# Kernel optimization log

Measured on AMD Instinct MI355X. Metric: run time of the kernel, lower is better.

## Reference

```python
import jax, jax.numpy as jnp
import numpy as np

IMG = 1024.0
MAXD = 8.0
EPS = 1e-6
ENC_HEADS = 12
DEC_HEADS = 16


def _ln(x, w, b):
    m = jnp.mean(x, -1, keepdims=True)
    v = jnp.mean((x - m) ** 2, -1, keepdims=True)
    return (x - m) / jnp.sqrt(v + EPS) * w + b


def _attn(x, qkv_w, qkv_b, pr_w, pr_b, nh, key_mask):
    B, L, D = x.shape
    hd = D // nh
    qkv = (x @ qkv_w + qkv_b).reshape(B, L, 3, nh, hd).transpose(2, 0, 3, 1, 4)
    q, k, v = qkv[0], qkv[1], qkv[2]  # [B, nh, L, hd]
    s = jnp.einsum('bhqd,bhkd->bhqk', q, k) * (hd ** -0.5)
    if key_mask is not None:
        # restrict attention to visible tokens; identical math to per-sample gather+encode
        s = jnp.where(key_mask[:, None, None, :], s, -1e9)
    a = jax.nn.softmax(s, -1)
    o = jnp.einsum('bhqk,bhkd->bhqd', a, v).transpose(0, 2, 1, 3).reshape(B, L, D)
    return o @ pr_w + pr_b


def _block(x, i, ln1w, ln1b, qkvw, qkvb, prw, prb, ln2w, ln2b, f1w, f1b, f2w, f2b, nh, key_mask):
    x = x + _attn(_ln(x, ln1w[i], ln1b[i]), qkvw[i], qkvb[i], prw[i], prb[i], nh, key_mask)
    h = jax.nn.gelu(_ln(x, ln2w[i], ln2b[i]) @ f1w[i] + f1b[i], approximate=False)
    return x + h @ f2w[i] + f2b[i]


def _pos(coords, depths, w1, b1, w2, b2):
    x1, x2, y1, y2 = coords[..., 0], coords[..., 1], coords[..., 2], coords[..., 3]
    f = jnp.stack([(x1 + x2) / 2.0 / IMG, (y1 + y2) / 2.0 / IMG,
                   (x2 - x1) / IMG, (y2 - y1) / IMG, depths / MAXD], -1)
    return jax.nn.gelu(f @ w1 + b1, approximate=False) @ w2 + b2


def _forward(patches, coords, depths, pe_w, pe_b, pos1_w, pos1_b, pos2_w, pos2_b,
             e_ln1_w, e_ln1_b, e_qkv_w, e_qkv_b, e_pr_w, e_pr_b, e_ln2_w, e_ln2_b,
             e_f1_w, e_f1_b, e_f2_w, e_f2_b, enorm_w, enorm_b,
             de_w, de_b, mask_token, dpos1_w, dpos1_b, dpos2_w, dpos2_b,
             d_ln1_w, d_ln1_b, d_qkv_w, d_qkv_b, d_pr_w, d_pr_b, d_ln2_w, d_ln2_b,
             d_f1_w, d_f1_b, d_f2_w, d_f2_b, dnorm_w, dnorm_b,
             hi_w, hi_b, hn_w, hn_b, mask):
    B, L = mask.shape
    x = patches.reshape(B, L, -1) @ pe_w + pe_b + _pos(coords, depths, pos1_w, pos1_b, pos2_w, pos2_b)
    visible = (mask == 0)
    h = x
    for i in range(e_qkv_w.shape[0]):
        h = _block(h, i, e_ln1_w, e_ln1_b, e_qkv_w, e_qkv_b, e_pr_w, e_pr_b,
                   e_ln2_w, e_ln2_b, e_f1_w, e_f1_b, e_f2_w, e_f2_b, ENC_HEADS, visible)
    encoded = jnp.where(visible[..., None], _ln(h, enorm_w, enorm_b), 0.0)
    xd = encoded @ de_w + de_b
    xd = jnp.where((mask != 0)[..., None], mask_token, xd)
    xd = xd + _pos(coords, depths, dpos1_w, dpos1_b, dpos2_w, dpos2_b)
    for i in range(d_qkv_w.shape[0]):
        xd = _block(xd, i, d_ln1_w, d_ln1_b, d_qkv_w, d_qkv_b, d_pr_w, d_pr_b,
                    d_ln2_w, d_ln2_b, d_f1_w, d_f1_b, d_f2_w, d_f2_b, DEC_HEADS, None)
    xd = _ln(xd, dnorm_w, dnorm_b)
    return (xd @ hi_w + hi_b, xd @ hn_w + hn_b)


def setup_inputs() -> dict:
    key = jax.random.key(0)
    ks = iter(jax.random.split(key, 80))
    def nrm(shape, std=0.02):
        return jax.random.normal(next(ks), shape, jnp.float32) * std
    B, L, P, C = 4, 512, 32, 1
    D, DD = 768, 512
    ED, DDEP = 12, 8
    pd = C * P * P
    inp = {}
    inp['patches'] = jax.random.normal(next(ks), (B, L, C, P, P), jnp.float32)
    inp['coords'] = jax.random.uniform(next(ks), (B, L, 4), jnp.float32)
    inp['depths'] = jax.random.uniform(next(ks), (B, L), jnp.float32)
    inp['mask'] = jax.random.randint(next(ks), (B, L), 0, 2, jnp.int32)
    inp['pe_w'] = nrm((pd, D)); inp['pe_b'] = jnp.zeros((D,))
    inp['pos1_w'] = nrm((5, D // 2)); inp['pos1_b'] = jnp.zeros((D // 2,))
    inp['pos2_w'] = nrm((D // 2, D)); inp['pos2_b'] = jnp.zeros((D,))
    inp['e_ln1_w'] = jnp.ones((ED, D)); inp['e_ln1_b'] = jnp.zeros((ED, D))
    inp['e_qkv_w'] = nrm((ED, D, 3 * D)); inp['e_qkv_b'] = jnp.zeros((ED, 3 * D))
    inp['e_pr_w'] = nrm((ED, D, D)); inp['e_pr_b'] = jnp.zeros((ED, D))
    inp['e_ln2_w'] = jnp.ones((ED, D)); inp['e_ln2_b'] = jnp.zeros((ED, D))
    inp['e_f1_w'] = nrm((ED, D, 4 * D)); inp['e_f1_b'] = jnp.zeros((ED, 4 * D))
    inp['e_f2_w'] = nrm((ED, 4 * D, D)); inp['e_f2_b'] = jnp.zeros((ED, D))
    inp['enorm_w'] = jnp.ones((D,)); inp['enorm_b'] = jnp.zeros((D,))
    inp['de_w'] = nrm((D, DD)); inp['de_b'] = jnp.zeros((DD,))
    inp['mask_token'] = nrm((DD,))
    inp['dpos1_w'] = nrm((5, DD // 2)); inp['dpos1_b'] = jnp.zeros((DD // 2,))
    inp['dpos2_w'] = nrm((DD // 2, DD)); inp['dpos2_b'] = jnp.zeros((DD,))
    inp['d_ln1_w'] = jnp.ones((DDEP, DD)); inp['d_ln1_b'] = jnp.zeros((DDEP, DD))
    inp['d_qkv_w'] = nrm((DDEP, DD, 3 * DD)); inp['d_qkv_b'] = jnp.zeros((DDEP, 3 * DD))
    inp['d_pr_w'] = nrm((DDEP, DD, DD)); inp['d_pr_b'] = jnp.zeros((DDEP, DD))
    inp['d_ln2_w'] = jnp.ones((DDEP, DD)); inp['d_ln2_b'] = jnp.zeros((DDEP, DD))
    inp['d_f1_w'] = nrm((DDEP, DD, 4 * DD)); inp['d_f1_b'] = jnp.zeros((DDEP, 4 * DD))
    inp['d_f2_w'] = nrm((DDEP, 4 * DD, DD)); inp['d_f2_b'] = jnp.zeros((DDEP, DD))
    inp['dnorm_w'] = jnp.ones((DD,)); inp['dnorm_b'] = jnp.zeros((DD,))
    inp['hi_w'] = nrm((DD, pd)); inp['hi_b'] = jnp.zeros((pd,))
    inp['hn_w'] = nrm((DD, pd)); inp['hn_b'] = jnp.zeros((pd,))
    return inp


def reference(patches, coords, depths, pe_w, pe_b, pos1_w, pos1_b, pos2_w, pos2_b,
              e_ln1_w, e_ln1_b, e_qkv_w, e_qkv_b, e_pr_w, e_pr_b, e_ln2_w, e_ln2_b,
              e_f1_w, e_f1_b, e_f2_w, e_f2_b, enorm_w, enorm_b,
              de_w, de_b, mask_token, dpos1_w, dpos1_b, dpos2_w, dpos2_b,
              d_ln1_w, d_ln1_b, d_qkv_w, d_qkv_b, d_pr_w, d_pr_b, d_ln2_w, d_ln2_b,
              d_f1_w, d_f1_b, d_f2_w, d_f2_b, dnorm_w, dnorm_b,
              hi_w, hi_b, hn_w, hn_b, mask):
    return _forward(patches, coords, depths, pe_w, pe_b, pos1_w, pos1_b, pos2_w, pos2_b,
                    e_ln1_w, e_ln1_b, e_qkv_w, e_qkv_b, e_pr_w, e_pr_b, e_ln2_w, e_ln2_b,
                    e_f1_w, e_f1_b, e_f2_w, e_f2_b, enorm_w, enorm_b,
                    de_w, de_b, mask_token, dpos1_w, dpos1_b, dpos2_w, dpos2_b,
                    d_ln1_w, d_ln1_b, d_qkv_w, d_qkv_b, d_pr_w, d_pr_b, d_ln2_w, d_ln2_b,
                    d_f1_w, d_f1_b, d_f2_w, d_f2_b, dnorm_w, dnorm_b,
                    hi_w, hi_b, hn_w, hn_b, mask)
```

## Files before the change

kernel.cpp:

```cpp
#include <hip/hip_runtime.h>
#include <hip/hip_bf16.h>

using bf16 = __hip_bfloat16;
typedef __bf16 bf16x8 __attribute__((ext_vector_type(8)));
typedef float f32x4 __attribute__((ext_vector_type(4)));

__device__ __forceinline__ float gelu_exact(float x) {
    return 0.5f * x * (1.0f + erff(x * 0.70710678118654752440f));
}

#define GLD_LDS16(g, l) __builtin_amdgcn_global_load_lds( \
    (__attribute__((address_space(1))) void*)(g),          \
    (__attribute__((address_space(3))) void*)(l), 16, 0, 0)

#define WAITV(n) asm volatile("s_waitcnt vmcnt(" #n ")" ::: "memory")

template<int BM,int BN,int WM,int WN,int FM,int FN,int OUT_BF16,int HAS_BIAS,int HAS_RES,int DO_GELU,int HEADS,int MPA,int OCC>
__global__ __launch_bounds__(256, OCC) void gemm_bt(
    const bf16* __restrict__ A, long lda,
    const bf16* __restrict__ Bt, long ldb,
    void* __restrict__ Cv, long ldc,
    const float* __restrict__ bias, const float* __restrict__ Res,
    int K, float alpha,
    const int* __restrict__ mpa_mask, const float* __restrict__ mpa_tok,
    const float* __restrict__ mpa_pos)
{
    static_assert(WM * WN == 4 && BM == WM * FM * 16 && BN == WN * FN * 16, "cfg");
    __shared__ alignas(16) unsigned short As[4][BM * 32];
    __shared__ alignas(16) unsigned short Bs[4][BN * 32];

    const int nwg = gridDim.x * gridDim.y;
    const int orig = blockIdx.y * gridDim.x + blockIdx.x;
    const int q = nwg >> 3, r = nwg & 7;
    const int xcd = orig & 7, seq = orig >> 3;
    const int wg = (xcd < r ? xcd * (q + 1) : r * (q + 1) + (xcd - r) * q) + seq;
    const int bn0 = (wg % gridDim.x) * BN;
    const int bm0 = (wg / gridDim.x) * BM;

    const int tid = threadIdx.x;
    const int wave = tid >> 6, lane = tid & 63;
    const int wm = (wave / WN) * (FM * 16);
    const int wn = (wave % WN) * (FN * 16);

    f32x4 acc[FM][FN] = {};

    constexpr int CA = BM / 16, CT = (BM + BN) / 16;
    constexpr int LPT = CT / 4;
    static_assert(CT % 4 == 0 && (LPT == 2 || LPT == 3), "stage cfg");
    const int lrow = lane >> 2;
    const int lcol = (((lane & 3) ^ ((lrow >> 1) & 3)) * 8);
    const int nk = K >> 5;

    const int fr = lane & 15;
    const int kg = lane >> 4;
    const int kswz = (kg ^ ((fr >> 1) & 3)) * 8;

    auto stage = [&](int buf, int kt) {
        const int k0 = kt * 32;
        for (int c = wave; c < CT; c += 4) {
            if (c < CA) {
                const bf16* src = A + (long)(bm0 + c * 16 + lrow) * lda + k0 + lcol;
                GLD_LDS16(src, &As[buf][c * 512]);
            } else {
                const int c2 = c - CA;
                const bf16* src = Bt + (long)(bn0 + c2 * 16 + lrow) * ldb + k0 + lcol;
                GLD_LDS16(src, &Bs[buf][c2 * 512]);
            }
        }
    };

    for (int i = 0; i < 4 && i < nk; ++i) stage(i, i);

    for (int t0 = 0; t0 < nk; t0 += 2) {
        const int c = (nk - t0 >= 2) ? 2 : 1;
        const int staged = (t0 + 4 < nk) ? (t0 + 4) : nk;
        const int extra = staged - (t0 + c);
        if constexpr (LPT == 2) {
            switch (extra) { case 2: WAITV(4); break; case 1: WAITV(2); break;
                             default: WAITV(0); }
        } else {
            switch (extra) { case 2: WAITV(6); break; case 1: WAITV(3); break;
                             default: WAITV(0); }
        }
        __builtin_amdgcn_s_barrier();
        __builtin_amdgcn_sched_barrier(0);

        #pragma unroll
        for (int u = 0; u < 2; ++u) {
            if (u == 1 && c == 1) break;
            const int cur = (t0 + u) & 3;
            bf16x8 af[FM], bfv[FN];
            #pragma unroll
            for (int m = 0; m < FM; ++m)
                af[m] = *(const bf16x8*)&As[cur][(wm + m * 16 + fr) * 32 + kswz];
            #pragma unroll
            for (int n = 0; n < FN; ++n)
                bfv[n] = *(const bf16x8*)&Bs[cur][(wn + n * 16 + fr) * 32 + kswz];
            __builtin_amdgcn_s_setprio(1);
            #pragma unroll
            for (int m = 0; m < FM; ++m)
                #pragma unroll
                for (int n = 0; n < FN; ++n)
                    acc[m][n] = __builtin_amdgcn_mfma_f32_16x16x32_bf16(af[m], bfv[n], acc[m][n], 0, 0, 0);
            __builtin_amdgcn_s_setprio(0);
        }

        __builtin_amdgcn_sched_barrier(0);
        asm volatile("s_waitcnt lgkmcnt(0)" ::: "memory");
        __builtin_amdgcn_s_barrier();
        if (t0 + 4 < nk) stage((t0 + 4) & 3, t0 + 4);
        if (t0 + 5 < nk) stage((t0 + 5) & 3, t0 + 5);
    }

    const int r0 = (lane >> 4) * 4;
    #pragma unroll
    for (int m = 0; m < FM; ++m) {
        const int rowb = bm0 + wm + m * 16 + r0;
        #pragma unroll
        for (int n = 0; n < FN; ++n) {
            const int col = bn0 + wn + n * 16 + fr;
            #pragma unroll
            for (int j = 0; j < 4; ++j) {
                float v = acc[m][n][j] * alpha;
                if (HEADS) {
                    v += (col < 1024) ? bias[col] : ((const float*)Res)[col - 1024];
                    const long idx = (col < 1024)
                        ? (long)(rowb + j) * 1024 + col
                        : 2097152L + (long)(rowb + j) * 1024 + (col - 1024);
                    ((float*)Cv)[idx] = v;
                    continue;
                }
                if (MPA) {
                    const int row = rowb + j;
                    v += bias[col];
                    if (mpa_mask[row] != 0) v = mpa_tok[col];
                    v += mpa_pos[(long)row * ldc + col];
                    ((float*)Cv)[(long)row * ldc + col] = v;
                    continue;
                }
                if (HAS_BIAS) v += bias[col];
                if (HAS_RES)  v += Res[(long)(rowb + j) * ldc + col];
                if (DO_GELU)  v = gelu_exact(v);
                const long idx = (long)(rowb + j) * ldc + col;
                if (OUT_BF16) ((bf16*)Cv)[idx] = __float2bfloat16(v);
                else          ((float*)Cv)[idx] = v;
            }
        }
    }
}

#define GEMM_A(OB,HB,HR,DG) gemm_bt<64,128,2,2,2,4, OB,HB,HR,DG,0,0,3>
#define GEMM_B(OB,HB,HR,DG) gemm_bt<64,64,2,2,2,2, OB,HB,HR,DG,0,0,4>
#define GEMM_H              gemm_bt<64,64,2,2,2,2, 0,1,0,0,1,0,4>
#define GEMM_M              gemm_bt<64,64,2,2,2,2, 0,1,0,0,0,1,4>

template<int HD, int MASKED>
__global__ __launch_bounds__(256) void flash_attn(
    const bf16* __restrict__ qkv, int ldq, int Doff, int nh,
    bf16* __restrict__ Out, int ldo,
    const int* __restrict__ mask, float alpha)
{
    constexpr int KVT = 256, KS = HD + 8, SV = KVT + 8;
    __shared__ unsigned short Ks[KVT * KS];
    __shared__ unsigned short Vs[HD * SV];
    __shared__ unsigned short Pl[4][16 * 40];

    const int bh = blockIdx.y, b = bh / nh, h = bh % nh;
    const int tid = threadIdx.x;
    const int wave = tid >> 6, lane = tid & 63;
    const int q0 = blockIdx.x * 64 + wave * 16;
    const int fr = lane & 15, kg = lane >> 4;

    const bf16* Qb = qkv + ((long)(b * 512 + q0 + fr)) * ldq + h * HD;
    bf16x8 af[HD / 32];
    #pragma unroll
    for (int kc = 0; kc < HD / 32; ++kc)
        af[kc] = *(const bf16x8*)(Qb + kc * 32 + kg * 8);

    const bf16* Kg = qkv + (long)b * 512 * ldq + Doff + h * HD;
    const bf16* Vg = qkv + (long)b * 512 * ldq + 2 * Doff + h * HD;
    const int* mg = mask + (long)b * 512;

    float m[4], l[4];
    f32x4 O[HD / 16] = {};
    #pragma unroll
    for (int j = 0; j < 4; ++j) { m[j] = -INFINITY; l[j] = 0.f; }

    for (int t = 0; t < 512; t += KVT) {
        __syncthreads();
        for (int i = tid; i < KVT * (HD / 8); i += 256) {
            const int rr = i / (HD / 8), c = i % (HD / 8);
            *(bf16x8*)&Ks[rr * KS + c * 8] = *(const bf16x8*)(Kg + (long)(t + rr) * ldq + c * 8);
        }
        for (int i = tid; i < KVT * (HD / 8); i += 256) {
            const int ll = i / (HD / 8), c = i % (HD / 8);
            bf16x8 vv = *(const bf16x8*)(Vg + (long)(t + ll) * ldq + c * 8);
            #pragma unroll
            for (int j = 0; j < 8; ++j) {
                bf16 e = ((const bf16*)&vv)[j];
                Vs[(c * 8 + j) * SV + ll] = *(unsigned short*)&e;
            }
        }
        __syncthreads();

        for (int n0 = 0; n0 < KVT; n0 += 32) {
            f32x4 s[2];
            int msk[2] = {0, 0};
            #pragma unroll
            for (int f = 0; f < 2; ++f) {
                f32x4 a = {};
                __builtin_amdgcn_s_setprio(1);
                #pragma unroll
                for (int kc = 0; kc < HD / 32; ++kc) {
                    bf16x8 kb = *(const bf16x8*)&Ks[(n0 + f * 16 + fr) * KS + kc * 32 + kg * 8];
                    a = __builtin_amdgcn_mfma_f32_16x16x32_bf16(af[kc], kb, a, 0, 0, 0);
                }
                __builtin_amdgcn_s_setprio(0);
                #pragma unroll
                for (int j = 0; j < 4; ++j) a[j] *= alpha;
                s[f] = a;
                if (MASKED) msk[f] = mg[t + n0 + f * 16 + fr];
            }
            float g[4], p0[4], p1[4];
            #pragma unroll
            for (int j = 0; j < 4; ++j) {
                float t4 = fmaxf(s[0][j], s[1][j]);
                t4 = fmaxf(t4, __shfl_xor(t4, 1));
                t4 = fmaxf(t4, __shfl_xor(t4, 2));
                t4 = fmaxf(t4, __shfl_xor(t4, 4));
                t4 = fmaxf(t4, __shfl_xor(t4, 8));
                const float mn = fmaxf(m[j], t4);
                g[j] = __expf(m[j] - mn);
                p0[j] = msk[0] ? 0.f : __expf(s[0][j] - mn);
                p1[j] = msk[1] ? 0.f : __expf(s[1][j] - mn);
                float rs = p0[j] + p1[j];
                rs += __shfl_xor(rs, 1);
                rs += __shfl_xor(rs, 2);
                rs += __shfl_xor(rs, 4);
                rs += __shfl_xor(rs, 8);
                l[j] = l[j] * g[j] + rs;
                m[j] = mn;
            }
            #pragma unroll
            for (int dt = 0; dt < HD / 16; ++dt)
                #pragma unroll
                for (int j = 0; j < 4; ++j) O[dt][j] *= g[j];
            unsigned short* pl = &Pl[wave][0];
            #pragma unroll
            for (int j = 0; j < 4; ++j) {
                bf16 b0 = __float2bfloat16(p0[j]);
                bf16 b1 = __float2bfloat16(p1[j]);
                pl[(kg * 4 + j) * 40 + fr]      = *(unsigned short*)&b0;
                pl[(kg * 4 + j) * 40 + 16 + fr] = *(unsigned short*)&b1;
            }
            __builtin_amdgcn_sched_barrier(0);
            bf16x8 pa = *(const bf16x8*)&pl[fr * 40 + kg * 8];
            __builtin_amdgcn_s_setprio(1);
            #pragma unroll
            for (int dt = 0; dt < HD / 16; ++dt) {
                bf16x8 vb = *(const bf16x8*)&Vs[(dt * 16 + fr) * SV + n0 + kg * 8];
                O[dt] = __builtin_amdgcn_mfma_f32_16x16x32_bf16(pa, vb, O[dt], 0, 0, 0);
            }
            __builtin_amdgcn_s_setprio(0);
        }
    }

    float inv[4];
    #pragma unroll
    for (int j = 0; j < 4; ++j) inv[j] = 1.0f / l[j];
    #pragma unroll
    for (int dt = 0; dt < HD / 16; ++dt)
        #pragma unroll
        for (int j = 0; j < 4; ++j) {
            const long row = (long)b * 512 + q0 + kg * 4 + j;
            Out[row * ldo + h * HD + dt * 16 + fr] = __float2bfloat16(O[dt][j] * inv[j]);
        }
}

__global__ void transpose_cast_b(const float* __restrict__ in, bf16* __restrict__ out,
                                 int K, int N, int Kpad, long inS, long outS)
{
    __shared__ float tile[32][33];
    in  += (long)blockIdx.z * inS;
    out += (long)blockIdx.z * outS;
    const int n0 = blockIdx.x * 32, k0 = blockIdx.y * 32;
    const int tx = threadIdx.x & 31, ty = threadIdx.x >> 5;
    #pragma unroll
    for (int r = 0; r < 4; ++r) {
        const int k = k0 + ty + r * 8, n = n0 + tx;
        tile[ty + r * 8][tx] = (k < K && n < N) ? in[(long)k * N + n] : 0.0f;
    }
    __syncthreads();
    #pragma unroll
    for (int r = 0; r < 4; ++r) {
        const int n = n0 + ty + r * 8, k = k0 + tx;
        if (n < N && k < Kpad)
            out[(long)n * Kpad + k] = __float2bfloat16(tile[tx][ty + r * 8]);
    }
}

template<int Dd, int MASKED>
__global__ __launch_bounds__(256) void ln_wave(
    const float* __restrict__ X, const float* __restrict__ w, const float* __restrict__ b,
    bf16* __restrict__ Y, const int* __restrict__ mask)
{
    const int wave = threadIdx.x >> 6, lane = threadIdx.x & 63;
    const int t = blockIdx.x * 4 + wave;
    const float* x = X + (long)t * Dd;
    constexpr int NE = Dd / 64;
    float v[NE];
    float s = 0.f, s2 = 0.f;
    #pragma unroll
    for (int k = 0; k < NE; ++k) {
        v[k] = x[lane + k * 64];
        s += v[k]; s2 += v[k] * v[k];
    }
    #pragma unroll
    for (int o = 32; o; o >>= 1) { s += __shfl_xor(s, o); s2 += __shfl_xor(s2, o); }
    const float mean = s / Dd;
    const float var = s2 / Dd - mean * mean;
    const float inv = 1.0f / sqrtf(var + 1e-6f);
    const bool zero = MASKED && (mask[t] != 0);
    #pragma unroll
    for (int k = 0; k < NE; ++k) {
        const int c = lane + k * 64;
        const float rr = zero ? 0.0f : ((v[k] - mean) * inv * w[c] + b[c]);
        Y[(long)t * Dd + c] = __float2bfloat16(rr);
    }
}

__global__ void build_feat(const float* __restrict__ coords, const float* __restrict__ depths,
                           bf16* __restrict__ F)
{
    const int t = blockIdx.x * 256 + threadIdx.x;
    if (t >= 2048) return;
    const float* c = coords + t * 4;
    float f[5];
    f[0] = (c[0] + c[1]) * 0.5f / 1024.0f;
    f[1] = (c[2] + c[3]) * 0.5f / 1024.0f;
    f[2] = (c[1] - c[0]) / 1024.0f;
    f[3] = (c[3] - c[2]) / 1024.0f;
    f[4] = depths[t] / 8.0f;
    bf16* o = F + (long)t * 32;
    #pragma unroll
    for (int j = 0; j < 32; ++j)
        o[j] = __float2bfloat16(j < 5 ? f[j] : 0.0f);
}

__global__ void conv_patches(const float* __restrict__ in, bf16* __restrict__ out, int n)
{
    const int i = blockIdx.x * 256 + threadIdx.x;
    if (i < n) out[i] = __float2bfloat16(in[i]);
}

extern "C" void kernel_launch(void* const* d_in, const int* in_sizes, int n_in,
                              void* d_out, int out_size, void* d_ws, size_t ws_size,
                              hipStream_t stream)
{
    (void)in_sizes; (void)n_in; (void)out_size;
    const int D = 768, DD = 512;

    const float* patches    = (const float*)d_in[0];
    const float* coords     = (const float*)d_in[1];
    const float* depths     = (const float*)d_in[2];
    const int*   mask       = (const int*)d_in[3];
    const float* pe_w       = (const float*)d_in[4];
    const float* pe_b       = (const float*)d_in[5];
    const float* pos1_w     = (const float*)d_in[6];
    const float* pos1_b     = (const float*)d_in[7];
    const float* pos2_w     = (const float*)d_in[8];
    const float* pos2_b     = (const float*)d_in[9];
    const float* e_ln1_w    = (const float*)d_in[10];
    const float* e_ln1_b    = (const float*)d_in[11];
    const float* e_qkv_w    = (const float*)d_in[12];
    const float* e_qkv_b    = (const float*)d_in[13];
    const float* e_pr_w     = (const float*)d_in[14];
    const float* e_pr_b     = (const float*)d_in[15];
    const float* e_ln2_w    = (const float*)d_in[16];
    const float* e_ln2_b    = (const float*)d_in[17];
    const float* e_f1_w     = (const float*)d_in[18];
    const float* e_f1_b     = (const float*)d_in[19];
    const float* e_f2_w     = (const float*)d_in[20];
    const float* e_f2_b     = (const float*)d_in[21];
    const float* enorm_w    = (const float*)d_in[22];
    const float* enorm_b    = (const float*)d_in[23];
    const float* de_w       = (const float*)d_in[24];
    const float* de_b       = (const float*)d_in[25];
    const float* mask_token = (const float*)d_in[26];
    const float* dpos1_w    = (const float*)d_in[27];
    const float* dpos1_b    = (const float*)d_in[28];
    const float* dpos2_w    = (const float*)d_in[29];
    const float* dpos2_b    = (const float*)d_in[30];
    const float* d_ln1_w    = (const float*)d_in[31];
    const float* d_ln1_b    = (const float*)d_in[32];
    const float* d_qkv_w    = (const float*)d_in[33];
    const float* d_qkv_b    = (const float*)d_in[34];
    const float* d_pr_w     = (const float*)d_in[35];
    const float* d_pr_b     = (const float*)d_in[36];
    const float* d_ln2_w    = (const float*)d_in[37];
    const float* d_ln2_b    = (const float*)d_in[38];
    const float* d_f1_w     = (const float*)d_in[39];
    const float* d_f1_b     = (const float*)d_in[40];
    const float* d_f2_w     = (const float*)d_in[41];
    const float* d_f2_b     = (const float*)d_in[42];
    const float* dnorm_w    = (const float*)d_in[43];
    const float* dnorm_b    = (const float*)d_in[44];
    const float* hi_w       = (const float*)d_in[45];
    const float* hi_b       = (const float*)d_in[46];
    const float* hn_w       = (const float*)d_in[47];
    const float* hn_b       = (const float*)d_in[48];

    char* p = (char*)d_ws;
    auto alloc = [&](size_t bytes) -> char* {
        char* r = p; p += (bytes + 255) & ~(size_t)255; return r;
    };
    bf16* pe_wt  = (bf16*)alloc(768L * 1024 * 2);
    bf16* pos1t  = (bf16*)alloc(384L * 32 * 2);
    bf16* pos2t  = (bf16*)alloc(768L * 384 * 2);
    bf16* dpos1t = (bf16*)alloc(256L * 32 * 2);
    bf16* dpos2t = (bf16*)alloc(512L * 256 * 2);
    bf16* de_t   = (bf16*)alloc(512L * 768 * 2);
    bf16* hi_t   = (bf16*)alloc(1024L * 512 * 2);
    bf16* hn_t   = (bf16*)alloc(1024L * 512 * 2);
    bf16* wslot  = (bf16*)alloc(3072L * 768 * 2);
    bf16*  feat    = (bf16*)alloc(2048L * 32 * 2);
    bf16*  patchbf = (bf16*)alloc(2048L * 1024 * 2);
    bf16*  poshE   = (bf16*)alloc(2048L * 384 * 2);
    float* posE    = (float*)alloc(2048L * 768 * 4);
    bf16*  poshD   = (bf16*)alloc(2048L * 256 * 2);
    float* posD    = (float*)alloc(2048L * 512 * 4);
    float* xbuf    = (float*)alloc(2048L * 768 * 4);
    bf16*  lnbuf   = (bf16*)alloc(2048L * 768 * 2);
    bf16*  qkvbuf  = (bf16*)alloc(2048L * 2304 * 2);
    bf16*  hid     = (bf16*)alloc(2048L * 3072 * 2);
    bf16*  pin     = (bf16*)alloc(2048L * 768 * 2);
    float* xd      = (float*)alloc(2048L * 512 * 4);

    const size_t bigBytes =
        (12L*2304*768 + 12L*768*768 + 12L*3072*768 + 12L*768*3072 +
          8L*1536*512 +  8L*512*512 +  8L*2048*512 +  8L*512*2048) * 2 + 8 * 256;
    const size_t used = (size_t)(p - (char*)d_ws);
    const bool batched = ws_size >= used + bigBytes;
    bf16 *eqkvt = nullptr, *eprt = nullptr, *ef1t = nullptr, *ef2t = nullptr;
    bf16 *dqkvt = nullptr, *dprt = nullptr, *df1t = nullptr, *df2t = nullptr;
    if (batched) {
        eqkvt = (bf16*)alloc(12L * 2304 * 768 * 2);
        eprt  = (bf16*)alloc(12L * 768 * 768 * 2);
        ef1t  = (bf16*)alloc(12L * 3072 * 768 * 2);
        ef2t  = (bf16*)alloc(12L * 768 * 3072 * 2);
        dqkvt = (bf16*)alloc(8L * 1536 * 512 * 2);
        dprt  = (bf16*)alloc(8L * 512 * 512 * 2);
        df1t  = (bf16*)alloc(8L * 2048 * 512 * 2);
        df2t  = (bf16*)alloc(8L * 512 * 2048 * 2);
    }

    conv_patches<<<8192, 256, 0, stream>>>(patches, patchbf, 2097152);
    build_feat<<<8, 256, 0, stream>>>(coords, depths, feat);

    auto trb = [&](const float* in, bf16* out, int K, int N, int Kpad, int z) {
        dim3 g((N + 31) / 32, (Kpad + 31) / 32, z);
        transpose_cast_b<<<g, 256, 0, stream>>>(in, out, K, N, Kpad, (long)K * N, (long)N * Kpad);
    };
    trb(pe_w,    pe_wt,  1024,  768, 1024, 1);
    trb(pos1_w,  pos1t,     5,  384,   32, 1);
    trb(pos2_w,  pos2t,   384,  768,  384, 1);
    trb(dpos1_w, dpos1t,    5,  256,   32, 1);
    trb(dpos2_w, dpos2t,  256,  512,  256, 1);
    trb(de_w,    de_t,    768,  512,  768, 1);
    trb(hi_w,    hi_t,    512, 1024,  512, 1);
    trb(hn_w,    hn_t,    512, 1024,  512, 1);
    if (batched) {
        trb(e_qkv_w, eqkvt, 768, 2304, 768, 12);
        trb(e_pr_w,  eprt,  768,  768, 768, 12);
        trb(e_f1_w,  ef1t,  768, 3072, 768, 12);
        trb(e_f2_w,  ef2t, 3072,  768, 3072, 12);
        trb(d_qkv_w, dqkvt, 512, 1536, 512, 8);
        trb(d_pr_w,  dprt,  512,  512, 512, 8);
        trb(d_f1_w,  df1t,  512, 2048, 512, 8);
        trb(d_f2_w,  df2t, 2048,  512, 2048, 8);
    }
    auto wsl = [&](const float* src, long off, int K, int N, int Kpad) -> const bf16* {
        dim3 g((N + 31) / 32, (Kpad + 31) / 32, 1);
        transpose_cast_b<<<g, 256, 0, stream>>>(src + off, wslot, K, N, Kpad, 0, 0);
        return wslot;
    };

    GEMM_B(1,1,0,1)<<<dim3(6,32,1),256,0,stream>>>(
        feat, 32, pos1t, 32, poshE, 384, pos1_b, nullptr, 32, 1.0f, nullptr, nullptr, nullptr);
    GEMM_B(0,1,0,0)<<<dim3(12,32,1),256,0,stream>>>(
        poshE, 384, pos2t, 384, posE, 768, pos2_b, nullptr, 384, 1.0f, nullptr, nullptr, nullptr);
    GEMM_B(1,1,0,1)<<<dim3(4,32,1),256,0,stream>>>(
        feat, 32, dpos1t, 32, poshD, 256, dpos1_b, nullptr, 32, 1.0f, nullptr, nullptr, nullptr);
    GEMM_B(0,1,0,0)<<<dim3(8,32,1),256,0,stream>>>(
        poshD, 256, dpos2t, 256, posD, 512, dpos2_b, nullptr, 256, 1.0f, nullptr, nullptr, nullptr);

    GEMM_B(0,1,1,0)<<<dim3(12,32,1),256,0,stream>>>(
        patchbf, 1024, pe_wt, 1024, xbuf, 768, pe_b, posE, 1024, 1.0f, nullptr, nullptr, nullptr);

    for (int i = 0; i < 12; ++i) {
        ln_wave<768,0><<<512,256,0,stream>>>(xbuf, e_ln1_w + i*D, e_ln1_b + i*D, lnbuf, nullptr);
        const bf16* Wq = batched ? eqkvt + (long)i*2304*768
                                 : wsl(e_qkv_w, (long)i*768*2304, 768, 2304, 768);
        GEMM_A(1,1,0,0)<<<dim3(18,32,1),256,0,stream>>>(
            lnbuf, 768, Wq, 768, qkvbuf, 2304, e_qkv_b + i*2304, nullptr, 768, 1.0f, nullptr, nullptr, nullptr);
        flash_attn<64,1><<<dim3(8,48),256,0,stream>>>(
            qkvbuf, 2304, 768, 12, pin, 768, mask, 0.125f);
        const bf16* Wp = batched ? eprt + (long)i*768*768
                                 : wsl(e_pr_w, (long)i*768*768, 768, 768, 768);
        GEMM_B(0,1,1,0)<<<dim3(12,32,1),256,0,stream>>>(
            pin, 768, Wp, 768, xbuf, 768, e_pr_b + i*768, xbuf, 768, 1.0f, nullptr, nullptr, nullptr);
        ln_wave<768,0><<<512,256,0,stream>>>(xbuf, e_ln2_w + i*D, e_ln2_b + i*D, lnbuf, nullptr);
        const bf16* W1 = batched ? ef1t + (long)i*3072*768
                                 : wsl(e_f1_w, (long)i*768*3072, 768, 3072, 768);
        GEMM_A(1,1,0,1)<<<dim3(24,32,1),256,0,stream>>>(
            lnbuf, 768, W1, 768, hid, 3072, e_f1_b + i*3072, nullptr, 768, 1.0f, nullptr, nullptr, nullptr);
        const bf16* W2 = batched ? ef2t + (long)i*768*3072
                                 : wsl(e_f2_w, (long)i*3072*768, 3072, 768, 3072);
        GEMM_B(0,1,1,0)<<<dim3(12,32,1),256,0,stream>>>(
            hid, 3072, W2, 3072, xbuf, 768, e_f2_b + i*768, xbuf, 3072, 1.0f, nullptr, nullptr, nullptr);
    }

    ln_wave<768,1><<<512,256,0,stream>>>(xbuf, enorm_w, enorm_b, lnbuf, mask);
    GEMM_M<<<dim3(8,32,1),256,0,stream>>>(
        lnbuf, 768, de_t, 768, xd, 512, de_b, nullptr, 768, 1.0f, mask, mask_token, posD);

    for (int i = 0; i < 8; ++i) {
        ln_wave<512,0><<<512,256,0,stream>>>(xd, d_ln1_w + i*DD, d_ln1_b + i*DD, lnbuf, nullptr);
        const bf16* Wq = batched ? dqkvt + (long)i*1536*512
                                 : wsl(d_qkv_w, (long)i*512*1536, 512, 1536, 512);
        GEMM_A(1,1,0,0)<<<dim3(12,32,1),256,0,stream>>>(
            lnbuf, 512, Wq, 512, qkvbuf, 1536, d_qkv_b + i*1536, nullptr, 512, 1.0f, nullptr, nullptr, nullptr);
        flash_attn<32,0><<<dim3(8,64),256,0,stream>>>(
            qkvbuf, 1536, 512, 16, pin, 512, nullptr, 0.17677669529663687f);
        const bf16* Wp = batched ? dprt + (long)i*512*512
                                 : wsl(d_pr_w, (long)i*512*512, 512, 512, 512);
        GEMM_B(0,1,1,0)<<<dim3(8,32,1),256,0,stream>>>(
            pin, 512, Wp, 512, xd, 512, d_pr_b + i*512, xd, 512, 1.0f, nullptr, nullptr, nullptr);
        ln_wave<512,0><<<512,256,0,stream>>>(xd, d_ln2_w + i*DD, d_ln2_b + i*DD, lnbuf, nullptr);
        const bf16* W1 = batched ? df1t + (long)i*2048*512
                                 : wsl(d_f1_w, (long)i*512*2048, 512, 2048, 512);
        GEMM_A(1,1,0,1)<<<dim3(16,32,1),256,0,stream>>>(
            lnbuf, 512, W1, 512, hid, 2048, d_f1_b + i*2048, nullptr, 512, 1.0f, nullptr, nullptr, nullptr);
        const bf16* W2 = batched ? df2t + (long)i*512*2048
                                 : wsl(d_f2_w, (long)i*2048*512, 2048, 512, 2048);
        GEMM_B(0,1,1,0)<<<dim3(8,32,1),256,0,stream>>>(
            hid, 2048, W2, 2048, xd, 512, d_f2_b + i*512, xd, 2048, 1.0f, nullptr, nullptr, nullptr);
    }

    ln_wave<512,0><<<512,256,0,stream>>>(xd, dnorm_w, dnorm_b, lnbuf, nullptr);
    GEMM_H<<<dim3(32,32,1),256,0,stream>>>(
        lnbuf, 512, hi_t, 512, (float*)d_out, 1024, hi_b, (const float*)hn_b, 512, 1.0f, nullptr, nullptr, nullptr);
}
```

Measured before the change: 2.838 ms.

## Split-K residual GEMMs with atomic accumulation into residual stream

```diff
diff --git a/kernel.cpp b/kernel.cpp
--- a/kernel.cpp
+++ b/kernel.cpp
@@ -15,7 +15,7 @@
 
 #define WAITV(n) asm volatile("s_waitcnt vmcnt(" #n ")" ::: "memory")
 
-template<int BM,int BN,int WM,int WN,int FM,int FN,int OUT_BF16,int HAS_BIAS,int HAS_RES,int DO_GELU,int HEADS,int MPA,int OCC>
+template<int BM,int BN,int WM,int WN,int FM,int FN,int OUT_BF16,int HAS_BIAS,int HAS_RES,int DO_GELU,int HEADS,int MPA,int OCC,int ATOM>
 __global__ __launch_bounds__(256, OCC) void gemm_bt(
     const bf16* __restrict__ A, long lda,
     const bf16* __restrict__ Bt, long ldb,
@@ -28,6 +28,11 @@
     static_assert(WM * WN == 4 && BM == WM * FM * 16 && BN == WN * FN * 16, "cfg");
     __shared__ alignas(16) unsigned short As[4][BM * 32];
     __shared__ alignas(16) unsigned short Bs[4][BN * 32];
+
+    if (ATOM) {
+        A  += (long)blockIdx.z * K;
+        Bt += (long)blockIdx.z * K;
+    }
 
     const int nwg = gridDim.x * gridDim.y;
     const int orig = blockIdx.y * gridDim.x + blockIdx.x;
@@ -122,6 +127,11 @@
             #pragma unroll
             for (int j = 0; j < 4; ++j) {
                 float v = acc[m][n][j] * alpha;
+                if (ATOM) {
+                    if (blockIdx.z == 0) v += bias[col];
+                    atomicAdd(&((float*)Cv)[(long)(rowb + j) * ldc + col], v);
+                    continue;
+                }
                 if (HEADS) {
                     v += (col < 1024) ? bias[col] : ((const float*)Res)[col - 1024];
                     const long idx = (col < 1024)
@@ -149,10 +159,11 @@
     }
 }
 
-#define GEMM_A(OB,HB,HR,DG) gemm_bt<64,128,2,2,2,4, OB,HB,HR,DG,0,0,3>
-#define GEMM_B(OB,HB,HR,DG) gemm_bt<64,64,2,2,2,2, OB,HB,HR,DG,0,0,4>
-#define GEMM_H              gemm_bt<64,64,2,2,2,2, 0,1,0,0,1,0,4>
-#define GEMM_M              gemm_bt<64,64,2,2,2,2, 0,1,0,0,0,1,4>
+#define GEMM_A(OB,HB,HR,DG) gemm_bt<64,128,2,2,2,4, OB,HB,HR,DG,0,0,3,0>
+#define GEMM_B(OB,HB,HR,DG) gemm_bt<64,64,2,2,2,2, OB,HB,HR,DG,0,0,4,0>
+#define GEMM_H              gemm_bt<64,64,2,2,2,2, 0,1,0,0,1,0,4,0>
+#define GEMM_M              gemm_bt<64,64,2,2,2,2, 0,1,0,0,0,1,4,0>
+#define GEMM_S              gemm_bt<64,64,2,2,2,2, 0,1,0,0,0,0,4,1>
 
 template<int HD, int MASKED>
 __global__ __launch_bounds__(256) void flash_attn(
@@ -507,8 +518,8 @@
             qkvbuf, 2304, 768, 12, pin, 768, mask, 0.125f);
         const bf16* Wp = batched ? eprt + (long)i*768*768
                                  : wsl(e_pr_w, (long)i*768*768, 768, 768, 768);
-        GEMM_B(0,1,1,0)<<<dim3(12,32,1),256,0,stream>>>(
-            pin, 768, Wp, 768, xbuf, 768, e_pr_b + i*768, xbuf, 768, 1.0f, nullptr, nullptr, nullptr);
+        GEMM_S<<<dim3(12,32,2),256,0,stream>>>(
+            pin, 768, Wp, 768, xbuf, 768, e_pr_b + i*768, nullptr, 384, 1.0f, nullptr, nullptr, nullptr);
         ln_wave<768,0><<<512,256,0,stream>>>(xbuf, e_ln2_w + i*D, e_ln2_b + i*D, lnbuf, nullptr);
         const bf16* W1 = batched ? ef1t + (long)i*3072*768
                                  : wsl(e_f1_w, (long)i*768*3072, 768, 3072, 768);
@@ -516,8 +527,8 @@
             lnbuf, 768, W1, 768, hid, 3072, e_f1_b + i*3072, nullptr, 768, 1.0f, nullptr, nullptr, nullptr);
         const bf16* W2 = batched ? ef2t + (long)i*768*3072
                                  : wsl(e_f2_w, (long)i*3072*768, 3072, 768, 3072);
-        GEMM_B(0,1,1,0)<<<dim3(12,32,1),256,0,stream>>>(
-            hid, 3072, W2, 3072, xbuf, 768, e_f2_b + i*768, xbuf, 3072, 1.0f, nullptr, nullptr, nullptr);
+        GEMM_S<<<dim3(12,32,2),256,0,stream>>>(
+            hid, 3072, W2, 3072, xbuf, 768, e_f2_b + i*768, nullptr, 1536, 1.0f, nullptr, nullptr, nullptr);
     }
 
     ln_wave<768,1><<<512,256,0,stream>>>(xbuf, enorm_w, enorm_b, lnbuf, mask);
@@ -534,8 +545,8 @@
             qkvbuf, 1536, 512, 16, pin, 512, nullptr, 0.17677669529663687f);
         const bf16* Wp = batched ? dprt + (long)i*512*512
                                  : wsl(d_pr_w, (long)i*512*512, 512, 512, 512);
-        GEMM_B(0,1,1,0)<<<dim3(8,32,1),256,0,stream>>>(
-            pin, 512, Wp, 512, xd, 512, d_pr_b + i*512, xd, 512, 1.0f, nullptr, nullptr, nullptr);
+        GEMM_S<<<dim3(8,32,2),256,0,stream>>>(
+            pin, 512, Wp, 512, xd, 512, d_pr_b + i*512, nullptr, 256, 1.0f, nullptr, nullptr, nullptr);
         ln_wave<512,0><<<512,256,0,stream>>>(xd, d_ln2_w + i*DD, d_ln2_b + i*DD, lnbuf, nullptr);
         const bf16* W1 = batched ? df1t + (long)i*2048*512
                                  : wsl(d_f1_w, (long)i*512*2048, 512, 2048, 512);
@@ -543,8 +554,8 @@
             lnbuf, 512, W1, 512, hid, 2048, d_f1_b + i*2048, nullptr, 512, 1.0f, nullptr, nullptr, nullptr);
         const bf16* W2 = batched ? df2t + (long)i*512*2048
                                  : wsl(d_f2_w, (long)i*2048*512, 2048, 512, 2048);
-        GEMM_B(0,1,1,0)<<<dim3(8,32,1),256,0,stream>>>(
-            hid, 2048, W2, 2048, xd, 512, d_f2_b + i*512, xd, 2048, 1.0f, nullptr, nullptr, nullptr);
+        GEMM_S<<<dim3(8,32,2),256,0,stream>>>(
+            hid, 2048, W2, 2048, xd, 512, d_f2_b + i*512, nullptr, 1024, 1.0f, nullptr, nullptr, nullptr);
     }
 
     ln_wave<512,0><<<512,256,0,stream>>>(xd, dnorm_w, dnorm_b, lnbuf, nullptr);
```

Measured after the change: 2.791 ms, median of 2. No clear change (-1.7%).
